# Kernel optimization log

Measured on AMD Instinct MI355X. Metric: run time of the kernel, lower is better.

The kernel has to match this reference:

```python
import jax, jax.numpy as jnp
import numpy as np

B, C_IN, C_OUT, H, W, K = 8, 64, 64, 128, 128, 3
KK = K * K


def _conv(x, w, b):
    # 3x3, stride 1, padding 1 (matches nn.Conv2d(stride=1, padding=1))
    y = jax.lax.conv_general_dilated(
        x, w, window_strides=(1, 1), padding=((1, 1), (1, 1)),
        dimension_numbers=('NCHW', 'OIHW', 'NCHW'))
    return y + b[None, :, None, None]


def setup_inputs() -> dict:
    key = jax.random.key(0)
    k1, k2, k3, k4, k5 = jax.random.split(key, 5)
    x = jax.random.normal(k1, (B, C_IN, H, W), jnp.float32)
    s = 1.0 / np.sqrt(C_IN * K * K)  # torch conv default init range
    w_off = jax.random.uniform(k2, (2 * KK, C_IN, K, K), jnp.float32, -s, s)
    b_off = jax.random.uniform(k3, (2 * KK,), jnp.float32, -s, s)
    w_reg = jax.random.uniform(k4, (C_OUT, C_IN, K, K), jnp.float32, -s, s)
    b_reg = jax.random.uniform(k5, (C_OUT,), jnp.float32, -s, s)
    return {"x": x, "w_off": w_off, "b_off": b_off, "w_reg": w_reg, "b_reg": b_reg}


def _deform_sample(x, offsets):
    # Equivalent of the K*K grid_sample(align_corners=True, padding_mode='zeros')
    # loop + sum over kernel positions. The norm/unnorm cancel, so sampling is
    # at absolute pixel coords base_grid + offsets.
    B_, C, H_, W_ = x.shape
    off = offsets.reshape(B_, KK, 2, H_, W_).transpose(0, 3, 4, 1, 2)  # B,H,W,KK,2
    xs = off[..., 0] + jnp.arange(W_, dtype=x.dtype)[None, None, :, None]
    ys = off[..., 1] + jnp.arange(H_, dtype=x.dtype)[None, :, None, None]
    x0 = jnp.floor(xs)
    y0 = jnp.floor(ys)
    wx1 = xs - x0
    wx0 = 1.0 - wx1
    wy1 = ys - y0
    wy0 = 1.0 - wy1
    x_flat = x.reshape(B_, C, H_ * W_)

    def gather(yi, xi, w):
        valid = (xi >= 0) & (xi < W_) & (yi >= 0) & (yi < H_)  # zeros padding
        xi_c = jnp.clip(xi, 0, W_ - 1).astype(jnp.int32)
        yi_c = jnp.clip(yi, 0, H_ - 1).astype(jnp.int32)
        idx = (yi_c * W_ + xi_c).reshape(B_, 1, H_ * W_ * KK)
        g = jnp.take_along_axis(
            x_flat, jnp.broadcast_to(idx, (B_, C, H_ * W_ * KK)), axis=2)
        g = g.reshape(B_, C, H_, W_, KK)
        wm = (w * valid.astype(x.dtype))[:, None]  # B,1,H,W,KK
        return (g * wm).sum(-1)  # sum over the KK kernel positions

    return (gather(y0, x0, wy0 * wx0)
            + gather(y0, x0 + 1.0, wy0 * wx1)
            + gather(y0 + 1.0, x0, wy1 * wx0)
            + gather(y0 + 1.0, x0 + 1.0, wy1 * wx1))


def reference(x, w_off, b_off, w_reg, b_reg):
    offsets = _conv(x, w_off, b_off)          # B, 2*KK, H, W
    sampled = _deform_sample(x, offsets)      # B, C, H, W (summed over KK)
    return _conv(sampled, w_reg, b_reg)       # B, C_OUT, H, W
```

## Files before the change

kernel.cpp:

```cpp
#include <hip/hip_runtime.h>

#define B_ 8
#define CIN 64
#define COUT 64
#define H_ 128
#define W_ 128
#define HW (H_*W_)
#define OFFP 24

typedef __attribute__((ext_vector_type(8))) short short8;
typedef __attribute__((ext_vector_type(4))) float f32x4;
typedef __attribute__((ext_vector_type(4))) unsigned uint4v;

__device__ __forceinline__ short f2bf(float f) {
    unsigned u = __float_as_uint(f);
    unsigned r = (u + 0x7fffu + ((u >> 16) & 1u)) >> 16;
    return (short)r;
}
__device__ __forceinline__ float bf2f(short s) {
    return __uint_as_float(((unsigned)(unsigned short)s) << 16);
}

template<int NT>
__device__ __forceinline__ void prep_one(const float* __restrict__ w, short* __restrict__ o,
                                         int i, int n_used) {
    int j = i & 7, lane = (i >> 3) & 63, rest = i >> 9;
    int nt = rest % NT, dc = rest / NT, c = dc & 1, d = dc >> 1;
    int oc = nt * 16 + (lane & 15);
    int ic = c * 32 + (lane >> 4) * 8 + j;
    float v = (oc < n_used) ? w[(oc * 64 + ic) * 9 + d] : 0.f;
    o[i] = f2bf(v);
}

__global__ __launch_bounds__(256) void k_prep(const float* __restrict__ wof,
                                              const float* __restrict__ wrg,
                                              short* __restrict__ wt1,
                                              short* __restrict__ wt2) {
    int i = blockIdx.x * 256 + threadIdx.x;
    if (i < 9 * 2 * 2 * 512) prep_one<2>(wof, wt1, i, 18);
    if (i < 9 * 2 * 4 * 512) prep_one<4>(wrg, wt2, i, 64);
}

__global__ __launch_bounds__(256) void k_tr(const float* __restrict__ x,
                                            short* __restrict__ xt) {
    __shared__ float tile[64 * 129];
    int bh = blockIdx.x;
    int bb = bh & 7, h = bh >> 3;
    const float* xp = x + (size_t)bb * (CIN * HW) + h * W_;
#pragma unroll
    for (int j = 0; j < 32; ++j) {
        int e = threadIdx.x + 256 * j;
        int cc = e >> 7, ww = e & 127;
        tile[cc * 129 + ww] = __builtin_nontemporal_load(xp + cc * HW + ww);
    }
    __syncthreads();
    short* op = xt + (((size_t)(bb << 7) + h) << 13);
#pragma unroll
    for (int j = 0; j < 32; ++j) {
        int e = threadIdx.x + 256 * j;
        int ww = e >> 6, cc = e & 63;
        op[e] = f2bf(tile[cc * 129 + ww]);
    }
}

template<int NT, bool TO_OFF>
__global__ __launch_bounds__(1024, 4) void k_conv(const short* __restrict__ src,
                                                  const short* __restrict__ wt,
                                                  const float* __restrict__ bias,
                                                  short* __restrict__ outb,
                                                  float* __restrict__ outf) {
    __shared__ short At[6 * 130 * 64];
    int blk = blockIdx.x;
    int bb = blk & 7;
    int h0 = (blk >> 3) << 2;

#pragma unroll
    for (int it = 0; it < 7; ++it) {
        int s = threadIdx.x + it * 1024;
        if (s < 6240) {
            int r = s / 1040, rem = s % 1040;
            int px = rem >> 3, ck = rem & 7;
            int y = h0 - 1 + r, xx = px - 1;
            bool v = ((unsigned)y < H_) && ((unsigned)xx < W_);
            int yc = min(max(y, 0), H_ - 1), xc = min(max(xx, 0), W_ - 1);
            short8 val = *(const short8*)(src + ((((size_t)(bb << 7) + yc) << 7) + xc) * 64 + ck * 8);
            short8 z = {0,0,0,0,0,0,0,0};
            if (!v) val = z;
            *(short8*)(&At[(r * 130 + px) * 64 + ((ck ^ (px & 7)) << 3)]) = val;
        }
    }
    __syncthreads();

    int lane = threadIdx.x & 63;
    int wave = threadIdx.x >> 6;
    int lr = wave >> 2;
    int p0 = (wave & 3) * 32;
    int m = lane & 15, quad = lane >> 4;

    f32x4 acc[2][NT];
#pragma unroll
    for (int nt = 0; nt < NT; ++nt) {
        int oc = nt * 16 + m;
        float bv = (!TO_OFF || oc < 18) ? bias[oc] : 0.f;
#pragma unroll
        for (int mt = 0; mt < 2; ++mt) {
            acc[mt][nt][0] = bv; acc[mt][nt][1] = bv;
            acc[mt][nt][2] = bv; acc[mt][nt][3] = bv;
        }
    }

#pragma unroll
    for (int d = 0; d < 9; ++d) {
        int dy = d / 3, dx = d % 3;
#pragma unroll
        for (int c = 0; c < 2; ++c) {
            short8 a[2];
#pragma unroll
            for (int mt = 0; mt < 2; ++mt) {
                int px = p0 + mt * 16 + m + dx;
                a[mt] = *(const short8*)(&At[((lr + dy) * 130 + px) * 64 + (((c * 4 + quad) ^ (px & 7)) << 3)]);
            }
#pragma unroll
            for (int nt = 0; nt < NT; ++nt) {
                short8 b = *(const short8*)(wt + ((((d * 2 + c) * NT + nt) * 64 + lane) << 3));
#pragma unroll
                for (int mt = 0; mt < 2; ++mt)
                    acc[mt][nt] = __builtin_amdgcn_mfma_f32_16x16x32_bf16(a[mt], b, acc[mt][nt], 0, 0, 0);
            }
        }
    }

    if (TO_OFF) {
        __syncthreads();
        unsigned short* St = (unsigned short*)At;
#pragma unroll
        for (int nt = 0; nt < NT; ++nt) {
            int oc = nt * 16 + m;
            if (oc < 20) {
#pragma unroll
                for (int mt = 0; mt < 2; ++mt) {
                    int pl = lr * 128 + p0 + mt * 16 + quad * 4;
#pragma unroll
                    for (int r = 0; r < 4; ++r)
                        St[(pl + r) * OFFP + oc] = (unsigned short)f2bf(acc[mt][nt][r]);
                }
            }
        }
        __syncthreads();
        const unsigned* Sd = (const unsigned*)St;
        unsigned* Od = (unsigned*)(outb + ((size_t)((bb << 14) + (h0 << 7))) * OFFP);
#pragma unroll
        for (int j = 0; j < 6; ++j)
            Od[threadIdx.x + 1024 * j] = Sd[threadIdx.x + 1024 * j];
    } else {
#pragma unroll
        for (int nt = 0; nt < NT; ++nt) {
            int oc = nt * 16 + m;
#pragma unroll
            for (int mt = 0; mt < 2; ++mt) {
                int wpix = p0 + mt * 16 + quad * 4;
                __builtin_nontemporal_store(acc[mt][nt],
                    (f32x4*)(outf + (((size_t)(bb * 64 + oc)) << 14) + ((h0 + lr) << 7) + wpix));
            }
        }
    }
}

__global__ __launch_bounds__(256, 2) void k_sample(const short* __restrict__ xt,
                                                   const short* __restrict__ offb,
                                                   short* __restrict__ smp) {
    int blk = blockIdx.x;
    int bb = blk & 7;
    int tile = blk >> 3;
    int tw = tile & 15, th = tile >> 4;
    int lp = threadIdx.x >> 3;
    int ck = threadIdx.x & 7;
    int w = (tw << 3) + (lp & 7);
    int h = (th << 2) + (lp >> 3);
    int pix = (bb << 14) + (h << 7) + w;
    const short* xb = xt + ((size_t)bb << 20) + ck * 8;

    const unsigned* op = (const unsigned*)(offb + (size_t)pix * OFFP);
    unsigned ow[9];
    {
        uint4v a = *(const uint4v*)op;
        uint4v bq = *(const uint4v*)(op + 4);
        ow[0]=a[0]; ow[1]=a[1]; ow[2]=a[2]; ow[3]=a[3];
        ow[4]=bq[0]; ow[5]=bq[1]; ow[6]=bq[2]; ow[7]=bq[3];
        ow[8]=op[8];
    }

    int  eoff[9][4];
    float wgt[9][4];
#pragma unroll
    for (int k = 0; k < 9; ++k) {
        float ox = bf2f((short)(ow[k] & 0xffff));
        float oy = bf2f((short)(ow[k] >> 16));
        float xs = (float)w + ox, ys = (float)h + oy;
        float x0f = floorf(xs), y0f = floorf(ys);
        float wx1 = xs - x0f, wx0 = 1.f - wx1;
        float wy1 = ys - y0f, wy0 = 1.f - wy1;
        int x0 = (int)x0f, y0 = (int)y0f;
        int x1 = x0 + 1, y1 = y0 + 1;
        int x0c = min(max(x0, 0), W_ - 1), x1c = min(max(x1, 0), W_ - 1);
        int y0c = min(max(y0, 0), H_ - 1), y1c = min(max(y1, 0), H_ - 1);
        bool vx0 = ((unsigned)x0 < W_), vx1 = ((unsigned)x1 < W_);
        bool vy0 = ((unsigned)y0 < H_), vy1 = ((unsigned)y1 < H_);
        wgt[k][0] = (vy0 && vx0) ? wy0 * wx0 : 0.f;
        wgt[k][1] = (vy0 && vx1) ? wy0 * wx1 : 0.f;
        wgt[k][2] = (vy1 && vx0) ? wy1 * wx0 : 0.f;
        wgt[k][3] = (vy1 && vx1) ? wy1 * wx1 : 0.f;
        eoff[k][0] = (y0c * W_ + x0c) << 6;
        eoff[k][1] = (y0c * W_ + x1c) << 6;
        eoff[k][2] = (y1c * W_ + x0c) << 6;
        eoff[k][3] = (y1c * W_ + x1c) << 6;
    }

    float acc[8];
#pragma unroll
    for (int i = 0; i < 8; ++i) acc[i] = 0.f;

#pragma unroll
    for (int g = 0; g < 3; ++g) {
        short8 v[3][4];
#pragma unroll
        for (int t = 0; t < 3; ++t)
#pragma unroll
            for (int n = 0; n < 4; ++n)
                v[t][n] = *(const short8*)(xb + eoff[g * 3 + t][n]);
#pragma unroll
        for (int t = 0; t < 3; ++t)
#pragma unroll
            for (int n = 0; n < 4; ++n) {
                float wv = wgt[g * 3 + t][n];
#pragma unroll
                for (int i = 0; i < 8; ++i)
                    acc[i] += wv * bf2f(v[t][n][i]);
            }
    }

    short8 o;
#pragma unroll
    for (int i = 0; i < 8; ++i) o[i] = f2bf(acc[i]);
    *(short8*)(smp + (size_t)pix * 64 + ck * 8) = o;
}

extern "C" void kernel_launch(void* const* d_in, const int* in_sizes, int n_in,
                              void* d_out, int out_size, void* d_ws, size_t ws_size,
                              hipStream_t stream) {
    const float* x   = (const float*)d_in[0];
    const float* wof = (const float*)d_in[1];
    const float* bof = (const float*)d_in[2];
    const float* wrg = (const float*)d_in[3];
    const float* brg = (const float*)d_in[4];
    float* out = (float*)d_out;

    char* ws = (char*)d_ws;
    short* xt   = (short*)ws;
    short* smp  = (short*)(ws + 16777216);
    short* offb = (short*)(ws + 2 * 16777216);
    short* wt1  = (short*)(ws + 2 * 16777216 + 6291456);
    short* wt2  = (short*)(ws + 2 * 16777216 + 6291456 + 36864);

    k_prep <<<dim3(144), 256, 0, stream>>>(wof, wrg, wt1, wt2);
    k_tr   <<<dim3(B_ * H_), 256, 0, stream>>>(x, xt);
    k_conv<2, true>  <<<dim3(B_ * H_ / 4), 1024, 0, stream>>>(xt, wt1, bof, offb, nullptr);
    k_sample<<<dim3((B_ * HW * 8) / 256), 256, 0, stream>>>(xt, offb, smp);
    k_conv<4, false> <<<dim3(B_ * H_ / 4), 1024, 0, stream>>>(smp, wt2, brg, nullptr, out);
}
```

Measured before the change: 151.7 us.

## Fold weight prep into transpose kernel and software-pipeline deform sampling gathers

Merges the weight-prep kernel into the transpose kernel, which removes one launch. In the sampling kernel, each block now stages its tile's offsets in shared memory with one coalesced load instead of per-thread strided loads. It then splits the nine kernel taps into three groups of three, double-buffered, so the gathers for the next group are issued before the current group is accumulated. The aim is to cut launch overhead and hide gather latency, at the cost of more registers (two 12-entry short8 buffers), which could hurt occupancy.

Result: faster. 147.5 us (-2.7%).

```diff
diff --git a/kernel.cpp b/kernel.cpp
--- a/kernel.cpp
+++ b/kernel.cpp
@@ -10,7 +10,6 @@
 
 typedef __attribute__((ext_vector_type(8))) short short8;
 typedef __attribute__((ext_vector_type(4))) float f32x4;
-typedef __attribute__((ext_vector_type(4))) unsigned uint4v;
 
 __device__ __forceinline__ short f2bf(float f) {
     unsigned u = __float_as_uint(f);
@@ -32,17 +31,16 @@
     o[i] = f2bf(v);
 }
 
-__global__ __launch_bounds__(256) void k_prep(const float* __restrict__ wof,
-                                              const float* __restrict__ wrg,
-                                              short* __restrict__ wt1,
-                                              short* __restrict__ wt2) {
+__global__ __launch_bounds__(256) void k_tr(const float* __restrict__ x,
+                                            short* __restrict__ xt,
+                                            const float* __restrict__ wof,
+                                            const float* __restrict__ wrg,
+                                            short* __restrict__ wt1,
+                                            short* __restrict__ wt2) {
     int i = blockIdx.x * 256 + threadIdx.x;
     if (i < 9 * 2 * 2 * 512) prep_one<2>(wof, wt1, i, 18);
     if (i < 9 * 2 * 4 * 512) prep_one<4>(wrg, wt2, i, 64);
-}
-
-__global__ __launch_bounds__(256) void k_tr(const float* __restrict__ x,
-                                            short* __restrict__ xt) {
+
     __shared__ float tile[64 * 129];
     int bh = blockIdx.x;
     int bb = bh & 7, h = bh >> 3;
@@ -166,36 +164,14 @@
     }
 }
 
-__global__ __launch_bounds__(256, 2) void k_sample(const short* __restrict__ xt,
-                                                   const short* __restrict__ offb,
-                                                   short* __restrict__ smp) {
-    int blk = blockIdx.x;
-    int bb = blk & 7;
-    int tile = blk >> 3;
-    int tw = tile & 15, th = tile >> 4;
-    int lp = threadIdx.x >> 3;
-    int ck = threadIdx.x & 7;
-    int w = (tw << 3) + (lp & 7);
-    int h = (th << 2) + (lp >> 3);
-    int pix = (bb << 14) + (h << 7) + w;
-    const short* xb = xt + ((size_t)bb << 20) + ck * 8;
-
-    const unsigned* op = (const unsigned*)(offb + (size_t)pix * OFFP);
-    unsigned ow[9];
-    {
-        uint4v a = *(const uint4v*)op;
-        uint4v bq = *(const uint4v*)(op + 4);
-        ow[0]=a[0]; ow[1]=a[1]; ow[2]=a[2]; ow[3]=a[3];
-        ow[4]=bq[0]; ow[5]=bq[1]; ow[6]=bq[2]; ow[7]=bq[3];
-        ow[8]=op[8];
-    }
-
-    int  eoff[9][4];
-    float wgt[9][4];
-#pragma unroll
-    for (int k = 0; k < 9; ++k) {
-        float ox = bf2f((short)(ow[k] & 0xffff));
-        float oy = bf2f((short)(ow[k] >> 16));
+__device__ __forceinline__ void prep3(const unsigned* __restrict__ myo, int g,
+                                      int w, int h, int cko,
+                                      int* __restrict__ eo, float* __restrict__ wg) {
+#pragma unroll
+    for (int t = 0; t < 3; ++t) {
+        unsigned owk = myo[g * 3 + t];
+        float ox = bf2f((short)(owk & 0xffff));
+        float oy = bf2f((short)(owk >> 16));
         float xs = (float)w + ox, ys = (float)h + oy;
         float x0f = floorf(xs), y0f = floorf(ys);
         float wx1 = xs - x0f, wx0 = 1.f - wx1;
@@ -206,43 +182,87 @@
         int y0c = min(max(y0, 0), H_ - 1), y1c = min(max(y1, 0), H_ - 1);
         bool vx0 = ((unsigned)x0 < W_), vx1 = ((unsigned)x1 < W_);
         bool vy0 = ((unsigned)y0 < H_), vy1 = ((unsigned)y1 < H_);
-        wgt[k][0] = (vy0 && vx0) ? wy0 * wx0 : 0.f;
-        wgt[k][1] = (vy0 && vx1) ? wy0 * wx1 : 0.f;
-        wgt[k][2] = (vy1 && vx0) ? wy1 * wx0 : 0.f;
-        wgt[k][3] = (vy1 && vx1) ? wy1 * wx1 : 0.f;
-        eoff[k][0] = (y0c * W_ + x0c) << 6;
-        eoff[k][1] = (y0c * W_ + x1c) << 6;
-        eoff[k][2] = (y1c * W_ + x0c) << 6;
-        eoff[k][3] = (y1c * W_ + x1c) << 6;
-    }
-
+        wg[t * 4 + 0] = (vy0 && vx0) ? wy0 * wx0 : 0.f;
+        wg[t * 4 + 1] = (vy0 && vx1) ? wy0 * wx1 : 0.f;
+        wg[t * 4 + 2] = (vy1 && vx0) ? wy1 * wx0 : 0.f;
+        wg[t * 4 + 3] = (vy1 && vx1) ? wy1 * wx1 : 0.f;
+        eo[t * 4 + 0] = ((y0c * W_ + x0c) << 6) + cko;
+        eo[t * 4 + 1] = ((y0c * W_ + x1c) << 6) + cko;
+        eo[t * 4 + 2] = ((y1c * W_ + x0c) << 6) + cko;
+        eo[t * 4 + 3] = ((y1c * W_ + x1c) << 6) + cko;
+    }
+}
+
+__global__ __launch_bounds__(256, 2) void k_sample(const short* __restrict__ xt,
+                                                   const short* __restrict__ offb,
+                                                   short* __restrict__ smp) {
+    __shared__ unsigned sow[4 * 96];
+    int blk = blockIdx.x;
+    int bb = blk & 7;
+    int tile = blk >> 3;
+    int tw = tile & 15, th = tile >> 4;
+
+    {
+        int rowid = threadIdx.x >> 6, rl = threadIdx.x & 63;
+        const unsigned* srcp = (const unsigned*)(offb +
+            ((size_t)((bb << 14) + (((th << 2) + rowid) << 7) + (tw << 3))) * OFFP);
+        sow[rowid * 96 + rl] = srcp[rl];
+        if (rl < 32) sow[rowid * 96 + 64 + rl] = srcp[64 + rl];
+    }
+    __syncthreads();
+
+    int lp = threadIdx.x >> 3;
+    int ck = threadIdx.x & 7;
+    int w = (tw << 3) + (lp & 7);
+    int h = (th << 2) + (lp >> 3);
+    int pix = (bb << 14) + (h << 7) + w;
+    const short* xim = xt + ((size_t)bb << 20);
+    int cko = ck * 8;
+    const unsigned* myo = &sow[(lp >> 3) * 96 + (lp & 7) * 12];
+
+    int eoffA[12], eoffB[12];
+    float wgtA[12], wgtB[12];
+    short8 vA[12], vB[12];
     float acc[8];
 #pragma unroll
     for (int i = 0; i < 8; ++i) acc[i] = 0.f;
 
-#pragma unroll
-    for (int g = 0; g < 3; ++g) {
-        short8 v[3][4];
-#pragma unroll
-        for (int t = 0; t < 3; ++t)
-#pragma unroll
-            for (int n = 0; n < 4; ++n)
-                v[t][n] = *(const short8*)(xb + eoff[g * 3 + t][n]);
-#pragma unroll
-        for (int t = 0; t < 3; ++t)
-#pragma unroll
-            for (int n = 0; n < 4; ++n) {
-                float wv = wgt[g * 3 + t][n];
-#pragma unroll
-                for (int i = 0; i < 8; ++i)
-                    acc[i] += wv * bf2f(v[t][n][i]);
-            }
+    prep3(myo, 0, w, h, cko, eoffA, wgtA);
+#pragma unroll
+    for (int n = 0; n < 12; ++n) vA[n] = *(const short8*)(xim + eoffA[n]);
+
+    prep3(myo, 1, w, h, cko, eoffB, wgtB);
+#pragma unroll
+    for (int n = 0; n < 12; ++n) vB[n] = *(const short8*)(xim + eoffB[n]);
+
+#pragma unroll
+    for (int n = 0; n < 12; ++n) {
+        float wv = wgtA[n];
+#pragma unroll
+        for (int i = 0; i < 8; ++i) acc[i] += wv * bf2f(vA[n][i]);
+    }
+
+    prep3(myo, 2, w, h, cko, eoffA, wgtA);
+#pragma unroll
+    for (int n = 0; n < 12; ++n) vA[n] = *(const short8*)(xim + eoffA[n]);
+
+#pragma unroll
+    for (int n = 0; n < 12; ++n) {
+        float wv = wgtB[n];
+#pragma unroll
+        for (int i = 0; i < 8; ++i) acc[i] += wv * bf2f(vB[n][i]);
+    }
+#pragma unroll
+    for (int n = 0; n < 12; ++n) {
+        float wv = wgtA[n];
+#pragma unroll
+        for (int i = 0; i < 8; ++i) acc[i] += wv * bf2f(vA[n][i]);
     }
 
     short8 o;
 #pragma unroll
     for (int i = 0; i < 8; ++i) o[i] = f2bf(acc[i]);
-    *(short8*)(smp + (size_t)pix * 64 + ck * 8) = o;
+    *(short8*)(smp + (size_t)pix * 64 + cko) = o;
 }
 
 extern "C" void kernel_launch(void* const* d_in, const int* in_sizes, int n_in,
@@ -262,8 +282,7 @@
     short* wt1  = (short*)(ws + 2 * 16777216 + 6291456);
     short* wt2  = (short*)(ws + 2 * 16777216 + 6291456 + 36864);
 
-    k_prep <<<dim3(144), 256, 0, stream>>>(wof, wrg, wt1, wt2);
-    k_tr   <<<dim3(B_ * H_), 256, 0, stream>>>(x, xt);
+    k_tr   <<<dim3(B_ * H_), 256, 0, stream>>>(x, xt, wof, wrg, wt1, wt2);
     k_conv<2, true>  <<<dim3(B_ * H_ / 4), 1024, 0, stream>>>(xt, wt1, bof, offb, nullptr);
     k_sample<<<dim3((B_ * HW * 8) / 256), 256, 0, stream>>>(xt, offb, smp);
     k_conv<4, false> <<<dim3(B_ * H_ / 4), 1024, 0, stream>>>(smp, wt2, brg, nullptr, out);
```
